# Kernel optimization log

Hardware: AMD Instinct MI355X
Metric: run time of the kernel (lower is better)

The kernel has to match this reference:

```python
import jax, jax.numpy as jnp
import numpy as np

TIME_STEPS = 4


def _kaiming(key, shape):
    # torch kaiming_normal_ default: std = sqrt(2 / fan_in), fan_in = shape[1]
    return jax.random.normal(key, shape, dtype=jnp.float32) * np.sqrt(2.0 / shape[1])


def setup_inputs() -> dict:
    key = jax.random.key(0)
    B, N, F, OUT = 8, 256, 64, 256
    ks = jax.random.split(key, 8)
    node_features = jax.random.normal(ks[0], (B, N, F), dtype=jnp.float32)
    adjacency_matrix = jax.random.randint(ks[1], (B, N, N), 0, 2, dtype=jnp.int32)
    w_graph_node_features = _kaiming(ks[2], (F, F))
    w_graph_neighbor_messages = _kaiming(ks[3], (F, F))
    u_graph_node_features = _kaiming(ks[4], (N, N))
    u_graph_neighbor_messages = _kaiming(ks[5], (F, F))
    fc_in = N * F
    bound = 1.0 / np.sqrt(fc_in)
    linear_w = jax.random.uniform(ks[6], (OUT, fc_in), minval=-bound, maxval=bound, dtype=jnp.float32)
    linear_b = jax.random.uniform(ks[7], (OUT,), minval=-bound, maxval=bound, dtype=jnp.float32)
    return {
        'node_features': node_features,
        'adjacency_matrix': adjacency_matrix,
        'w_graph_node_features': w_graph_node_features,
        'w_graph_neighbor_messages': w_graph_neighbor_messages,
        'u_graph_node_features': u_graph_node_features,
        'u_graph_neighbor_messages': u_graph_neighbor_messages,
        'linear_w': linear_w,
        'linear_b': linear_b,
        'batch_size': B,
    }


def reference(node_features, adjacency_matrix, w_graph_node_features,
              w_graph_neighbor_messages, u_graph_node_features,
              u_graph_neighbor_messages, linear_w, linear_b, batch_size):
    X = node_features                      # [B,N,F]
    B, N, F = X.shape
    mask = (adjacency_matrix != 0).astype(X.dtype)  # [B,N,N]; mask[b,i,k]=1 if k is a neighbor of i
    # base[b,i] = W_nf @ x[i]  (sent by node i to every neighbor)
    base = jnp.einsum('fg,big->bif', w_graph_node_features, X)
    # messages M[b,a,c] = message from node a to node c, shape [B,N,N,F]
    M = jnp.zeros((B, N, N, F), dtype=X.dtype)
    for _ in range(TIME_STEPS):
        # T[b,k,i] = W_nm @ M[k,i]   (transformed incoming message from k to i)
        T = jnp.einsum('fg,bkig->bkif', w_graph_neighbor_messages, M)
        # S[b,i] = sum over neighbors k of i of T[b,k,i]
        S = jnp.einsum('bik,bkif->bif', mask, T)
        # message i->j excludes the message that came from j: S[i] - T[j,i]
        Tt = jnp.swapaxes(T, 1, 2)         # Tt[b,i,j] = T[b,j,i]
        M = jax.nn.relu(base[:, :, None, :] + S[:, :, None, :] - Tt) * mask[..., None]
    # encode: torch sums messages[node_id] over dim 0, i.e. sum_j M[i,j]
    agg = M.sum(axis=2)                    # [B,N,F]
    enc = jax.nn.relu(
        jnp.einsum('nm,bmf->bnf', u_graph_node_features, X)
        + jnp.einsum('fg,big->bif', u_graph_neighbor_messages, agg)
    )
    flat = enc.reshape(B, N * F)
    return jax.nn.sigmoid(flat @ linear_w.T + linear_b)
```

## Files before the change

### kernel.cpp

```cpp
#include <hip/hip_runtime.h>
#include <hip/hip_bf16.h>
#include <math.h>

#define B 8
#define N 256
#define F 64
#define OUTD 256
typedef unsigned long long u64;
typedef __attribute__((ext_vector_type(8))) short bf16x8;
typedef __attribute__((ext_vector_type(4))) float f32x4;

__device__ __forceinline__ void build_frag(const float* v8, bf16x8& h, bf16x8& l) {
#pragma unroll
    for (int j = 0; j < 8; ++j) {
        unsigned u = __float_as_uint(v8[j]);
        unsigned hb = u & 0xffff0000u;
        float r = v8[j] - __uint_as_float(hb);
        h[j] = (short)(hb >> 16);
        l[j] = (short)(__float_as_uint(r) >> 16);
    }
}

__global__ __launch_bounds__(256) void pack_rows_kernel(const int* __restrict__ adj,
                                                        u64* __restrict__ rowbits) {
    int b = blockIdx.y;
    int i = blockIdx.x * 4 + (threadIdx.x >> 6);
    int lane = threadIdx.x & 63;
#pragma unroll
    for (int wd = 0; wd < 4; ++wd) {
        int v = adj[(long)(b * N + i) * N + wd * 64 + lane];
        u64 bits = __ballot(v != 0);
        if (lane == 0) rowbits[(b * N + i) * 4 + wd] = bits;
    }
}

__global__ __launch_bounds__(256) void pack_cols_kernel(const u64* __restrict__ rowbits,
                                                        u64* __restrict__ colbits) {
    int b = blockIdx.y;
    int i = blockIdx.x * 4 + (threadIdx.x >> 6);
    int lane = threadIdx.x & 63;
    int iw = i >> 6, ib = i & 63;
#pragma unroll
    for (int wd = 0; wd < 4; ++wd) {
        u64 rv = rowbits[(b * N + wd * 64 + lane) * 4 + iw];
        u64 bits = __ballot((rv >> ib) & 1ull);
        if (lane == 0) colbits[(b * N + i) * 4 + wd] = bits;
    }
}

__global__ __launch_bounds__(64) void prep_kernel(const float* __restrict__ X,
                                                  const float* __restrict__ Wnf,
                                                  const float* __restrict__ Wnm,
                                                  float* __restrict__ base,
                                                  float* __restrict__ P) {
    int bi = blockIdx.x;
    int f = threadIdx.x;
    __shared__ float xs[F];
    __shared__ float rs[F];
    xs[f] = X[bi * F + f];
    __syncthreads();
    float acc = 0.f;
#pragma unroll
    for (int g = 0; g < F; ++g) acc += Wnf[f * F + g] * xs[g];
    base[bi * F + f] = acc;
    rs[f] = fmaxf(acc, 0.f);
    __syncthreads();
    float acc2 = 0.f;
#pragma unroll
    for (int g = 0; g < F; ++g) acc2 += Wnm[f * F + g] * rs[g];
    P[bi * F + f] = acc2;
}

__global__ __launch_bounds__(256) void v2_kernel(const float* __restrict__ base,
                                                 const float* __restrict__ P,
                                                 const u64* __restrict__ rowbits,
                                                 const u64* __restrict__ colbits,
                                                 float* __restrict__ V2) {
    int i = blockIdx.x, b = blockIdx.y;
    int t = threadIdx.x, w = t >> 6, f = t & 63;
    int bi = b * N + i;
    __shared__ float red[4][F];
    u64 both = rowbits[bi * 4 + w] & colbits[bi * 4 + w];
    const float* Pb = P + (size_t)b * N * F;
    float acc = 0.f;
    for (int j = 0; j < 64; ++j) {
        float mk = ((both >> j) & 1ull) ? 1.f : 0.f;
        acc += mk * Pb[(w * 64 + j) * F + f];
    }
    red[w][f] = acc;
    __syncthreads();
    if (t < F) V2[bi * F + t] = base[bi * F + t] + red[0][t] + red[1][t] + red[2][t] + red[3][t];
}

__global__ __launch_bounds__(256) void s3_kernel(const float* __restrict__ base,
                                                 const float* __restrict__ P,
                                                 const float* __restrict__ V2g,
                                                 const u64* __restrict__ rowbits,
                                                 const u64* __restrict__ colbits,
                                                 const float* __restrict__ Wnm,
                                                 float* __restrict__ V3) {
    int i = blockIdx.x, b = blockIdx.y;
    int t = threadIdx.x, w = t >> 6, f = t & 63;
    int bi = b * N + i;
    __shared__ float red[4][F];
    __shared__ float ubuf[F];
    u64 both = rowbits[bi * 4 + w] & colbits[bi * 4 + w];
    float pif = P[(size_t)bi * F + f];
    const float* Vb = V2g + (size_t)b * N * F;
    float acc = 0.f;
    for (int j = 0; j < 64; ++j) {
        float mk = ((both >> j) & 1ull) ? 1.f : 0.f;
        acc += mk * fmaxf(Vb[(w * 64 + j) * F + f] - pif, 0.f);
    }
    red[w][f] = acc;
    __syncthreads();
    if (t < F) ubuf[t] = red[0][t] + red[1][t] + red[2][t] + red[3][t];
    __syncthreads();
    if (w == 0) {
        float u = ubuf[f];
        float wrow[F];
        const float4* wr = (const float4*)(Wnm + (size_t)f * F);
#pragma unroll
        for (int q = 0; q < 16; ++q) *(float4*)&wrow[q * 4] = wr[q];
        float a = 0.f;
#pragma unroll
        for (int g = 0; g < F; ++g) a = fmaf(wrow[g], __shfl(u, g, 64), a);
        V3[bi * F + f] = base[bi * F + f] + a;
    }
}

__global__ __launch_bounds__(256, 1) void bigstep_kernel(
        const float* __restrict__ base,
        const float* __restrict__ P,
        const float* __restrict__ V2g,
        const float* __restrict__ V3,
        const u64* __restrict__ rowbits,
        const u64* __restrict__ colbits,
        const float* __restrict__ Wnm,
        float* __restrict__ agg) {
    int i = blockIdx.x, b = blockIdx.y;
    int t = threadIdx.x;
    int w = t >> 6, l = t & 63;
    int ln = l & 15, grp = l >> 4;
    int bi = b * N + i;
    int bN = b * N;
    __shared__ float m2lds[4][64][68];
    __shared__ float red[4][F];
    __shared__ float v4buf[F];

    u64 rw = rowbits[bi * 4 + w];
    u64 cw = colbits[bi * 4 + w];
    u64 bothw = rw & cw;

    bf16x8 Ah[8], Al[8];
#pragma unroll
    for (int ft = 0; ft < 4; ++ft) {
        const float4* wr = (const float4*)(Wnm + (size_t)(16 * ft + ln) * F);
#pragma unroll
        for (int ks = 0; ks < 2; ++ks) {
            float e[8];
            *(float4*)&e[0] = wr[8 * ks + 2 * grp];
            *(float4*)&e[4] = wr[8 * ks + 2 * grp + 1];
            build_frag(e, Ah[ft * 2 + ks], Al[ft * 2 + ks]);
        }
    }
    float v2f[2][8];
    {
        const float4* vr = (const float4*)(V2g + (size_t)bi * F);
#pragma unroll
        for (int ks = 0; ks < 2; ++ks) {
            *(float4*)&v2f[ks][0] = vr[8 * ks + 2 * grp];
            *(float4*)&v2f[ks][4] = vr[8 * ks + 2 * grp + 1];
        }
    }

    f32x4 acc1[4][4];
#pragma unroll
    for (int ft = 0; ft < 4; ++ft)
#pragma unroll
        for (int kt = 0; kt < 4; ++kt) acc1[ft][kt] = (f32x4){0.f, 0.f, 0.f, 0.f};

#pragma unroll
    for (int kt = 0; kt < 4; ++kt) {
        int kglob = w * 64 + kt * 16 + ln;
        const float4* pr = (const float4*)(P + (size_t)(bN + kglob) * F);
#pragma unroll
        for (int ks = 0; ks < 2; ++ks) {
            float e[8];
            *(float4*)&e[0] = pr[8 * ks + 2 * grp];
            *(float4*)&e[4] = pr[8 * ks + 2 * grp + 1];
#pragma unroll
            for (int j = 0; j < 8; ++j) e[j] = fmaxf(v2f[ks][j] - e[j], 0.f);
            bf16x8 Bh, Bl;
            build_frag(e, Bh, Bl);
#pragma unroll
            for (int ft = 0; ft < 4; ++ft) {
                acc1[ft][kt] = __builtin_amdgcn_mfma_f32_16x16x32_bf16(Ah[ft * 2 + ks], Bh, acc1[ft][kt], 0, 0, 0);
                acc1[ft][kt] = __builtin_amdgcn_mfma_f32_16x16x32_bf16(Ah[ft * 2 + ks], Bl, acc1[ft][kt], 0, 0, 0);
                acc1[ft][kt] = __builtin_amdgcn_mfma_f32_16x16x32_bf16(Al[ft * 2 + ks], Bh, acc1[ft][kt], 0, 0, 0);
            }
        }
    }

#pragma unroll
    for (int kt = 0; kt < 4; ++kt) {
        int kloc = kt * 16 + ln;
        int kglob = w * 64 + kloc;
        float km = ((bothw >> kloc) & 1ull) ? 1.f : 0.f;
        const float* v3r = V3 + (size_t)(bN + kglob) * F;
#pragma unroll
        for (int ft = 0; ft < 4; ++ft) {
            int g0 = 16 * ft + 4 * grp;
            float4 v3v = *(const float4*)(v3r + g0);
            f32x4 tq = acc1[ft][kt];
            float4 m2v;
            m2v.x = km * fmaxf(v3v.x - tq[0], 0.f);
            m2v.y = km * fmaxf(v3v.y - tq[1], 0.f);
            m2v.z = km * fmaxf(v3v.z - tq[2], 0.f);
            m2v.w = km * fmaxf(v3v.w - tq[3], 0.f);
            *(float4*)&m2lds[w][kloc][g0] = m2v;
        }
    }

    f32x4 acc2[4][4];
#pragma unroll
    for (int ft = 0; ft < 4; ++ft)
#pragma unroll
        for (int kt = 0; kt < 4; ++kt) acc2[ft][kt] = (f32x4){0.f, 0.f, 0.f, 0.f};

#pragma unroll
    for (int kt = 0; kt < 4; ++kt) {
        int kloc = kt * 16 + ln;
#pragma unroll
        for (int ks = 0; ks < 2; ++ks) {
            int g0 = 32 * ks + 8 * grp;
            float e[8];
            *(float4*)&e[0] = *(const float4*)&m2lds[w][kloc][g0];
            *(float4*)&e[4] = *(const float4*)&m2lds[w][kloc][g0 + 4];
            bf16x8 Bh, Bl;
            build_frag(e, Bh, Bl);
#pragma unroll
            for (int ft = 0; ft < 4; ++ft) {
                acc2[ft][kt] = __builtin_amdgcn_mfma_f32_16x16x32_bf16(Ah[ft * 2 + ks], Bh, acc2[ft][kt], 0, 0, 0);
                acc2[ft][kt] = __builtin_amdgcn_mfma_f32_16x16x32_bf16(Ah[ft * 2 + ks], Bl, acc2[ft][kt], 0, 0, 0);
                acc2[ft][kt] = __builtin_amdgcn_mfma_f32_16x16x32_bf16(Al[ft * 2 + ks], Bh, acc2[ft][kt], 0, 0, 0);
            }
        }
    }

    float s4[4][4];
#pragma unroll
    for (int ft = 0; ft < 4; ++ft)
#pragma unroll
        for (int r = 0; r < 4; ++r)
            s4[ft][r] = acc2[ft][0][r] + acc2[ft][1][r] + acc2[ft][2][r] + acc2[ft][3][r];
#pragma unroll
    for (int m = 1; m <= 8; m <<= 1)
#pragma unroll
        for (int ft = 0; ft < 4; ++ft)
#pragma unroll
            for (int r = 0; r < 4; ++r)
                s4[ft][r] += __shfl_xor(s4[ft][r], m, 64);
    if (ln == 0) {
#pragma unroll
        for (int ft = 0; ft < 4; ++ft) {
            float4 q = make_float4(s4[ft][0], s4[ft][1], s4[ft][2], s4[ft][3]);
            *(float4*)&red[w][16 * ft + 4 * grp] = q;
        }
    }
    __syncthreads();
    if (t < F) v4buf[t] = base[(size_t)bi * F + t] + red[0][t] + red[1][t] + red[2][t] + red[3][t];
    __syncthreads();

    float v4r[4][4];
#pragma unroll
    for (int ft = 0; ft < 4; ++ft) {
        float4 q = *(const float4*)&v4buf[16 * ft + 4 * grp];
        v4r[ft][0] = q.x; v4r[ft][1] = q.y; v4r[ft][2] = q.z; v4r[ft][3] = q.w;
    }
    float av[4][4];
#pragma unroll
    for (int ft = 0; ft < 4; ++ft)
#pragma unroll
        for (int r = 0; r < 4; ++r) av[ft][r] = 0.f;
#pragma unroll
    for (int kt = 0; kt < 4; ++kt) {
        float rbm = ((rw >> (kt * 16 + ln)) & 1ull) ? 1.f : 0.f;
#pragma unroll
        for (int ft = 0; ft < 4; ++ft)
#pragma unroll
            for (int r = 0; r < 4; ++r)
                av[ft][r] += rbm * fmaxf(v4r[ft][r] - acc2[ft][kt][r], 0.f);
    }
#pragma unroll
    for (int m = 1; m <= 8; m <<= 1)
#pragma unroll
        for (int ft = 0; ft < 4; ++ft)
#pragma unroll
            for (int r = 0; r < 4; ++r)
                av[ft][r] += __shfl_xor(av[ft][r], m, 64);
    if (ln == 0) {
#pragma unroll
        for (int ft = 0; ft < 4; ++ft) {
            float4 q = make_float4(av[ft][0], av[ft][1], av[ft][2], av[ft][3]);
            *(float4*)&red[w][16 * ft + 4 * grp] = q;
        }
    }
    __syncthreads();
    if (t < F) agg[(size_t)bi * F + t] = red[0][t] + red[1][t] + red[2][t] + red[3][t];
}

__global__ __launch_bounds__(256) void encode_kernel(const float* __restrict__ X,
                                                     const float* __restrict__ Unf,
                                                     const float* __restrict__ Unm,
                                                     const float* __restrict__ agg,
                                                     float* __restrict__ enc) {
    int n = blockIdx.x, b = blockIdx.y;
    int t = threadIdx.x, w = t >> 6, f = t & 63;
    __shared__ float red[4][F];
    const float* urow = Unf + (size_t)n * N;
    const float* Xb = X + (size_t)b * N * F;
    float acc = 0.f;
    for (int j = 0; j < 64; ++j) {
        int m = w * 64 + j;
        acc += urow[m] * Xb[m * F + f];
    }
    red[w][f] = acc;
    __syncthreads();
    if (w == 0) {
        float msum = red[0][f] + red[1][f] + red[2][f] + red[3][f];
        float ag = agg[((size_t)b * N + n) * F + f];
        float wrow[F];
        const float4* wr = (const float4*)(Unm + (size_t)f * F);
#pragma unroll
        for (int q = 0; q < 16; ++q) *(float4*)&wrow[q * 4] = wr[q];
        float a = 0.f;
#pragma unroll
        for (int g = 0; g < F; ++g) a = fmaf(wrow[g], __shfl(ag, g, 64), a);
        enc[((size_t)b * N + n) * F + f] = fmaxf(msum + a, 0.f);
    }
}

__global__ __launch_bounds__(256) void final_kernel(const float* __restrict__ enc,
                                                    const float* __restrict__ lw,
                                                    const float* __restrict__ lb,
                                                    float* __restrict__ out) {
    int o = blockIdx.x;
    int t = threadIdx.x;
    float acc[B];
#pragma unroll
    for (int b = 0; b < B; ++b) acc[b] = 0.f;
    const float4* lrow = (const float4*)(lw + (size_t)o * (N * F));
    const float4* e4 = (const float4*)enc;
    for (int k = t; k < (N * F) / 4; k += 256) {
        float4 wv = lrow[k];
#pragma unroll
        for (int b = 0; b < B; ++b) {
            float4 ev = e4[b * (N * F / 4) + k];
            acc[b] += wv.x * ev.x + wv.y * ev.y + wv.z * ev.z + wv.w * ev.w;
        }
    }
    __shared__ float red[B][256];
#pragma unroll
    for (int b = 0; b < B; ++b) red[b][t] = acc[b];
    __syncthreads();
    for (int off = 128; off > 0; off >>= 1) {
        if (t < off) {
#pragma unroll
            for (int b = 0; b < B; ++b) red[b][t] += red[b][t + off];
        }
        __syncthreads();
    }
    if (t < B) {
        float z = red[t][0] + lb[o];
        out[t * OUTD + o] = 1.f / (1.f + expf(-z));
    }
}

extern "C" void kernel_launch(void* const* d_in, const int* in_sizes, int n_in,
                              void* d_out, int out_size, void* d_ws, size_t ws_size,
                              hipStream_t stream) {
    const float* X   = (const float*)d_in[0];
    const int*   adj = (const int*)d_in[1];
    const float* Wnf = (const float*)d_in[2];
    const float* Wnm = (const float*)d_in[3];
    const float* Unf = (const float*)d_in[4];
    const float* Unm = (const float*)d_in[5];
    const float* lw  = (const float*)d_in[6];
    const float* lb  = (const float*)d_in[7];
    float* out = (float*)d_out;

    const long BNF = (long)B * N * F;
    u64* rowbits = (u64*)d_ws;
    u64* colbits = rowbits + (long)B * N * 4;
    float* fws = (float*)(colbits + (long)B * N * 4);
    float* base = fws;          fws += BNF;
    float* P    = fws;          fws += BNF;
    float* V2   = fws;          fws += BNF;
    float* V3   = fws;          fws += BNF;
    float* aggp = fws;          fws += BNF;
    float* enc  = fws;          fws += BNF;
    (void)ws_size; (void)in_sizes; (void)n_in; (void)out_size;

    pack_rows_kernel<<<dim3(N / 4, B), 256, 0, stream>>>(adj, rowbits);
    pack_cols_kernel<<<dim3(N / 4, B), 256, 0, stream>>>(rowbits, colbits);
    prep_kernel<<<B * N, F, 0, stream>>>(X, Wnf, Wnm, base, P);
    v2_kernel<<<dim3(N, B), 256, 0, stream>>>(base, P, rowbits, colbits, V2);
    s3_kernel<<<dim3(N, B), 256, 0, stream>>>(base, P, V2, rowbits, colbits, Wnm, V3);
    bigstep_kernel<<<dim3(N, B), 256, 0, stream>>>(base, P, V2, V3, rowbits, colbits, Wnm, aggp);
    encode_kernel<<<dim3(N, B), 256, 0, stream>>>(X, Unf, Unm, aggp, enc);
    final_kernel<<<OUTD, 256, 0, stream>>>(enc, lw, lb, out);
}
```

Before: 121.6 us.

## Merge prep kernels, fold column packing into v2, and shrink bigstep LDS footprint

Row-bit packing and the base/P matvec prep now share one launch, and column-bit packing is computed inside the v2 kernel, cutting the launch count from eight to six. The bigstep kernel interleaves the two MFMA stages per k-tile, so its LDS staging buffer shrinks to a quarter and launch bounds allow four blocks per CU instead of one. The s3 and encode kernels spread the final 64x64 matvec across all four waves with an LDS reduction instead of using a single wave. The intent is to cut launch overhead and raise occupancy, at the cost of an extra barrier and reduction step in s3 and encode.

```diff
diff --git a/kernel.cpp b/kernel.cpp
--- a/kernel.cpp
+++ b/kernel.cpp
@@ -21,67 +21,56 @@
     }
 }
 
-__global__ __launch_bounds__(256) void pack_rows_kernel(const int* __restrict__ adj,
-                                                        u64* __restrict__ rowbits) {
+__global__ __launch_bounds__(256) void prepA_kernel(const int* __restrict__ adj,
+                                                    const float* __restrict__ X,
+                                                    const float* __restrict__ Wnf,
+                                                    const float* __restrict__ Wnm,
+                                                    u64* __restrict__ rowbits,
+                                                    float* __restrict__ base,
+                                                    float* __restrict__ P) {
     int b = blockIdx.y;
-    int i = blockIdx.x * 4 + (threadIdx.x >> 6);
+    int w = threadIdx.x >> 6;
     int lane = threadIdx.x & 63;
-#pragma unroll
-    for (int wd = 0; wd < 4; ++wd) {
-        int v = adj[(long)(b * N + i) * N + wd * 64 + lane];
-        u64 bits = __ballot(v != 0);
-        if (lane == 0) rowbits[(b * N + i) * 4 + wd] = bits;
-    }
-}
-
-__global__ __launch_bounds__(256) void pack_cols_kernel(const u64* __restrict__ rowbits,
-                                                        u64* __restrict__ colbits) {
-    int b = blockIdx.y;
-    int i = blockIdx.x * 4 + (threadIdx.x >> 6);
-    int lane = threadIdx.x & 63;
-    int iw = i >> 6, ib = i & 63;
-#pragma unroll
-    for (int wd = 0; wd < 4; ++wd) {
-        u64 rv = rowbits[(b * N + wd * 64 + lane) * 4 + iw];
-        u64 bits = __ballot((rv >> ib) & 1ull);
-        if (lane == 0) colbits[(b * N + i) * 4 + wd] = bits;
-    }
-}
-
-__global__ __launch_bounds__(64) void prep_kernel(const float* __restrict__ X,
-                                                  const float* __restrict__ Wnf,
-                                                  const float* __restrict__ Wnm,
-                                                  float* __restrict__ base,
-                                                  float* __restrict__ P) {
-    int bi = blockIdx.x;
-    int f = threadIdx.x;
-    __shared__ float xs[F];
-    __shared__ float rs[F];
-    xs[f] = X[bi * F + f];
-    __syncthreads();
-    float acc = 0.f;
-#pragma unroll
-    for (int g = 0; g < F; ++g) acc += Wnf[f * F + g] * xs[g];
-    base[bi * F + f] = acc;
-    rs[f] = fmaxf(acc, 0.f);
-    __syncthreads();
-    float acc2 = 0.f;
-#pragma unroll
-    for (int g = 0; g < F; ++g) acc2 += Wnm[f * F + g] * rs[g];
-    P[bi * F + f] = acc2;
-}
-
-__global__ __launch_bounds__(256) void v2_kernel(const float* __restrict__ base,
-                                                 const float* __restrict__ P,
-                                                 const u64* __restrict__ rowbits,
-                                                 const u64* __restrict__ colbits,
-                                                 float* __restrict__ V2) {
+    if (blockIdx.x < 64) {
+        int i = blockIdx.x * 4 + w;
+#pragma unroll
+        for (int wd = 0; wd < 4; ++wd) {
+            int v = adj[(long)(b * N + i) * N + wd * 64 + lane];
+            u64 bits = __ballot(v != 0);
+            if (lane == 0) rowbits[(b * N + i) * 4 + wd] = bits;
+        }
+    } else {
+        int n = (blockIdx.x - 64) * 4 + w;
+        int bi = b * N + n;
+        float x = X[(size_t)bi * F + lane];
+        float acc = 0.f;
+#pragma unroll
+        for (int g = 0; g < F; ++g) acc = fmaf(Wnf[lane * F + g], __shfl(x, g, 64), acc);
+        base[(size_t)bi * F + lane] = acc;
+        float rs = fmaxf(acc, 0.f);
+        float acc2 = 0.f;
+#pragma unroll
+        for (int g = 0; g < F; ++g) acc2 = fmaf(Wnm[lane * F + g], __shfl(rs, g, 64), acc2);
+        P[(size_t)bi * F + lane] = acc2;
+    }
+}
+
+__global__ __launch_bounds__(256) void v2B_kernel(const float* __restrict__ base,
+                                                  const float* __restrict__ P,
+                                                  const u64* __restrict__ rowbits,
+                                                  u64* __restrict__ colbits,
+                                                  float* __restrict__ V2) {
     int i = blockIdx.x, b = blockIdx.y;
     int t = threadIdx.x, w = t >> 6, f = t & 63;
     int bi = b * N + i;
+    int bN = b * N;
+    int iw = i >> 6, ib = i & 63;
     __shared__ float red[4][F];
-    u64 both = rowbits[bi * 4 + w] & colbits[bi * 4 + w];
-    const float* Pb = P + (size_t)b * N * F;
+    u64 rv = rowbits[(bN + w * 64 + f) * 4 + iw];
+    u64 cw = __ballot((rv >> ib) & 1ull);
+    if (f == 0) colbits[bi * 4 + w] = cw;
+    u64 both = cw & rowbits[bi * 4 + w];
+    const float* Pb = P + (size_t)bN * F;
     float acc = 0.f;
     for (int j = 0; j < 64; ++j) {
         float mk = ((both >> j) & 1ull) ? 1.f : 0.f;
@@ -89,7 +78,7 @@
     }
     red[w][f] = acc;
     __syncthreads();
-    if (t < F) V2[bi * F + t] = base[bi * F + t] + red[0][t] + red[1][t] + red[2][t] + red[3][t];
+    if (t < F) V2[(size_t)bi * F + t] = base[(size_t)bi * F + t] + red[0][t] + red[1][t] + red[2][t] + red[3][t];
 }
 
 __global__ __launch_bounds__(256) void s3_kernel(const float* __restrict__ base,
@@ -103,7 +92,6 @@
     int t = threadIdx.x, w = t >> 6, f = t & 63;
     int bi = b * N + i;
     __shared__ float red[4][F];
-    __shared__ float ubuf[F];
     u64 both = rowbits[bi * 4 + w] & colbits[bi * 4 + w];
     float pif = P[(size_t)bi * F + f];
     const float* Vb = V2g + (size_t)b * N * F;
@@ -114,22 +102,21 @@
     }
     red[w][f] = acc;
     __syncthreads();
-    if (t < F) ubuf[t] = red[0][t] + red[1][t] + red[2][t] + red[3][t];
-    __syncthreads();
-    if (w == 0) {
-        float u = ubuf[f];
-        float wrow[F];
-        const float4* wr = (const float4*)(Wnm + (size_t)f * F);
-#pragma unroll
-        for (int q = 0; q < 16; ++q) *(float4*)&wrow[q * 4] = wr[q];
-        float a = 0.f;
-#pragma unroll
-        for (int g = 0; g < F; ++g) a = fmaf(wrow[g], __shfl(u, g, 64), a);
-        V3[bi * F + f] = base[bi * F + f] + a;
-    }
-}
-
-__global__ __launch_bounds__(256, 1) void bigstep_kernel(
+    float u = red[0][f] + red[1][f] + red[2][f] + red[3][f];
+    __syncthreads();
+    float wv[16];
+    const float4* wr = (const float4*)(Wnm + (size_t)f * F + 16 * w);
+#pragma unroll
+    for (int q = 0; q < 4; ++q) *(float4*)&wv[q * 4] = wr[q];
+    float a = 0.f;
+#pragma unroll
+    for (int q = 0; q < 16; ++q) a = fmaf(wv[q], __shfl(u, 16 * w + q, 64), a);
+    red[w][f] = a;
+    __syncthreads();
+    if (t < F) V3[(size_t)bi * F + t] = base[(size_t)bi * F + t] + red[0][t] + red[1][t] + red[2][t] + red[3][t];
+}
+
+__global__ __launch_bounds__(256, 4) void bigstep_kernel(
         const float* __restrict__ base,
         const float* __restrict__ P,
         const float* __restrict__ V2g,
@@ -144,7 +131,7 @@
     int ln = l & 15, grp = l >> 4;
     int bi = b * N + i;
     int bN = b * N;
-    __shared__ float m2lds[4][64][68];
+    __shared__ float m2lds[4][16][68];
     __shared__ float red[4][F];
     __shared__ float v4buf[F];
 
@@ -174,15 +161,18 @@
         }
     }
 
-    f32x4 acc1[4][4];
+    f32x4 acc2[4][4];
 #pragma unroll
     for (int ft = 0; ft < 4; ++ft)
 #pragma unroll
-        for (int kt = 0; kt < 4; ++kt) acc1[ft][kt] = (f32x4){0.f, 0.f, 0.f, 0.f};
+        for (int kt = 0; kt < 4; ++kt) acc2[ft][kt] = (f32x4){0.f, 0.f, 0.f, 0.f};
 
 #pragma unroll
     for (int kt = 0; kt < 4; ++kt) {
         int kglob = w * 64 + kt * 16 + ln;
+        f32x4 acc1[4];
+#pragma unroll
+        for (int ft = 0; ft < 4; ++ft) acc1[ft] = (f32x4){0.f, 0.f, 0.f, 0.f};
         const float4* pr = (const float4*)(P + (size_t)(bN + kglob) * F);
 #pragma unroll
         for (int ks = 0; ks < 2; ++ks) {
@@ -195,48 +185,33 @@
             build_frag(e, Bh, Bl);
 #pragma unroll
             for (int ft = 0; ft < 4; ++ft) {
-                acc1[ft][kt] = __builtin_amdgcn_mfma_f32_16x16x32_bf16(Ah[ft * 2 + ks], Bh, acc1[ft][kt], 0, 0, 0);
-                acc1[ft][kt] = __builtin_amdgcn_mfma_f32_16x16x32_bf16(Ah[ft * 2 + ks], Bl, acc1[ft][kt], 0, 0, 0);
-                acc1[ft][kt] = __builtin_amdgcn_mfma_f32_16x16x32_bf16(Al[ft * 2 + ks], Bh, acc1[ft][kt], 0, 0, 0);
+                acc1[ft] = __builtin_amdgcn_mfma_f32_16x16x32_bf16(Ah[ft * 2 + ks], Bh, acc1[ft], 0, 0, 0);
+                acc1[ft] = __builtin_amdgcn_mfma_f32_16x16x32_bf16(Ah[ft * 2 + ks], Bl, acc1[ft], 0, 0, 0);
+                acc1[ft] = __builtin_amdgcn_mfma_f32_16x16x32_bf16(Al[ft * 2 + ks], Bh, acc1[ft], 0, 0, 0);
             }
         }
-    }
-
-#pragma unroll
-    for (int kt = 0; kt < 4; ++kt) {
-        int kloc = kt * 16 + ln;
-        int kglob = w * 64 + kloc;
-        float km = ((bothw >> kloc) & 1ull) ? 1.f : 0.f;
-        const float* v3r = V3 + (size_t)(bN + kglob) * F;
-#pragma unroll
-        for (int ft = 0; ft < 4; ++ft) {
-            int g0 = 16 * ft + 4 * grp;
-            float4 v3v = *(const float4*)(v3r + g0);
-            f32x4 tq = acc1[ft][kt];
-            float4 m2v;
-            m2v.x = km * fmaxf(v3v.x - tq[0], 0.f);
-            m2v.y = km * fmaxf(v3v.y - tq[1], 0.f);
-            m2v.z = km * fmaxf(v3v.z - tq[2], 0.f);
-            m2v.w = km * fmaxf(v3v.w - tq[3], 0.f);
-            *(float4*)&m2lds[w][kloc][g0] = m2v;
-        }
-    }
-
-    f32x4 acc2[4][4];
-#pragma unroll
-    for (int ft = 0; ft < 4; ++ft)
-#pragma unroll
-        for (int kt = 0; kt < 4; ++kt) acc2[ft][kt] = (f32x4){0.f, 0.f, 0.f, 0.f};
-
-#pragma unroll
-    for (int kt = 0; kt < 4; ++kt) {
-        int kloc = kt * 16 + ln;
+        {
+            float km = ((bothw >> (kt * 16 + ln)) & 1ull) ? 1.f : 0.f;
+            const float* v3r = V3 + (size_t)(bN + kglob) * F;
+#pragma unroll
+            for (int ft = 0; ft < 4; ++ft) {
+                int g0 = 16 * ft + 4 * grp;
+                float4 v3v = *(const float4*)(v3r + g0);
+                f32x4 tq = acc1[ft];
+                float4 m2v;
+                m2v.x = km * fmaxf(v3v.x - tq[0], 0.f);
+                m2v.y = km * fmaxf(v3v.y - tq[1], 0.f);
+                m2v.z = km * fmaxf(v3v.z - tq[2], 0.f);
+                m2v.w = km * fmaxf(v3v.w - tq[3], 0.f);
+                *(float4*)&m2lds[w][ln][g0] = m2v;
+            }
+        }
 #pragma unroll
         for (int ks = 0; ks < 2; ++ks) {
             int g0 = 32 * ks + 8 * grp;
             float e[8];
-            *(float4*)&e[0] = *(const float4*)&m2lds[w][kloc][g0];
-            *(float4*)&e[4] = *(const float4*)&m2lds[w][kloc][g0 + 4];
+            *(float4*)&e[0] = *(const float4*)&m2lds[w][ln][g0];
+            *(float4*)&e[4] = *(const float4*)&m2lds[w][ln][g0 + 4];
             bf16x8 Bh, Bl;
             build_frag(e, Bh, Bl);
 #pragma unroll
@@ -327,18 +302,20 @@
     }
     red[w][f] = acc;
     __syncthreads();
-    if (w == 0) {
-        float msum = red[0][f] + red[1][f] + red[2][f] + red[3][f];
-        float ag = agg[((size_t)b * N + n) * F + f];
-        float wrow[F];
-        const float4* wr = (const float4*)(Unm + (size_t)f * F);
-#pragma unroll
-        for (int q = 0; q < 16; ++q) *(float4*)&wrow[q * 4] = wr[q];
-        float a = 0.f;
-#pragma unroll
-        for (int g = 0; g < F; ++g) a = fmaf(wrow[g], __shfl(ag, g, 64), a);
-        enc[((size_t)b * N + n) * F + f] = fmaxf(msum + a, 0.f);
-    }
+    float msum = red[0][f] + red[1][f] + red[2][f] + red[3][f];
+    __syncthreads();
+    float ag = agg[((size_t)b * N + n) * F + f];
+    float wv[16];
+    const float4* wr = (const float4*)(Unm + (size_t)f * F + 16 * w);
+#pragma unroll
+    for (int q = 0; q < 4; ++q) *(float4*)&wv[q * 4] = wr[q];
+    float a = 0.f;
+#pragma unroll
+    for (int q = 0; q < 16; ++q) a = fmaf(wv[q], __shfl(ag, 16 * w + q, 64), a);
+    red[w][f] = a;
+    __syncthreads();
+    if (w == 0)
+        enc[((size_t)b * N + n) * F + f] = fmaxf(msum + red[0][f] + red[1][f] + red[2][f] + red[3][f], 0.f);
 }
 
 __global__ __launch_bounds__(256) void final_kernel(const float* __restrict__ enc,
@@ -402,10 +379,8 @@
     float* enc  = fws;          fws += BNF;
     (void)ws_size; (void)in_sizes; (void)n_in; (void)out_size;
 
-    pack_rows_kernel<<<dim3(N / 4, B), 256, 0, stream>>>(adj, rowbits);
-    pack_cols_kernel<<<dim3(N / 4, B), 256, 0, stream>>>(rowbits, colbits);
-    prep_kernel<<<B * N, F, 0, stream>>>(X, Wnf, Wnm, base, P);
-    v2_kernel<<<dim3(N, B), 256, 0, stream>>>(base, P, rowbits, colbits, V2);
+    prepA_kernel<<<dim3(64 + 64, B), 256, 0, stream>>>(adj, X, Wnf, Wnm, rowbits, base, P);
+    v2B_kernel<<<dim3(N, B), 256, 0, stream>>>(base, P, rowbits, colbits, V2);
     s3_kernel<<<dim3(N, B), 256, 0, stream>>>(base, P, V2, rowbits, colbits, Wnm, V3);
     bigstep_kernel<<<dim3(N, B), 256, 0, stream>>>(base, P, V2, V3, rowbits, colbits, Wnm, aggp);
     encode_kernel<<<dim3(N, B), 256, 0, stream>>>(X, Unf, Unm, aggp, enc);
```

Measured after the change: 183.7 us. +51.0%, slower.
